# Kernel tuning notes

Hardware: AMD Instinct MI355X
Metric: run time of the kernel (lower is better)

Reference implementation:

```python
import jax, jax.numpy as jnp
import numpy as np

NUM_ITERATIONS = 3
EPS = 1e-8


def squash(s):
    # Hinton squash over the pose dims (last two axes). s: [b, C, os0, os1]
    sq_norm = jnp.sum(s * s, axis=(-2, -1), keepdims=True)
    norm = jnp.sqrt(sq_norm + EPS)
    return (sq_norm / (1.0 + sq_norm)) * (s / norm)


def setup_inputs() -> dict:
    key = jax.random.key(0)
    k1, k2, k3 = jax.random.split(key, 3)
    b, B, H, W = 256, 32, 6, 6
    C, os0, is0 = 10, 16, 16
    input_caps_poses = jax.random.normal(k1, (b, B, H, W, is0, 1), dtype=jnp.float32)
    input_caps_activations = jax.random.uniform(k2, (b, B, H, W), dtype=jnp.float32)
    # weight: [input_caps_types, kh, kw, output_caps_types, os0, is0], std=0.1
    weight = 0.1 * jax.random.normal(k3, (B, H, W, C, os0, is0), dtype=jnp.float32)
    # routing_bias: [C, oh=1, ow=1, os0, os1] initialized to 0.1
    routing_bias = jnp.full((C, 1, 1, os0, 1), 0.1, dtype=jnp.float32)
    return {
        "input_caps_poses": input_caps_poses,
        "input_caps_activations": input_caps_activations,
        "weight": weight,
        "routing_bias": routing_bias,
    }


def reference(input_caps_poses, input_caps_activations, weight, routing_bias):
    # Votes: per input capsule (type B, spatial h,w), transform pose [is0,1]
    # by W[B,h,w,C,os0,is0] -> vote [os0,1] for each output type C.
    # votes: [b, C, B, H, W, os0, os1]
    votes = jnp.einsum('Bhwcoi,bBhwij->bcBhwoj', weight, input_caps_poses)
    b, C, B, H, W, os0, os1 = votes.shape
    bias = routing_bias.reshape(C, os0, os1)  # oh=ow=1

    # Dynamic routing-by-agreement. logits: [b, C, B, H, W]
    logits = jnp.zeros((b, C, B, H, W), dtype=votes.dtype)
    v = None
    c = None
    for it in range(NUM_ITERATIONS):
        c = jax.nn.softmax(logits, axis=1)  # coupling over output types C
        s = jnp.einsum('bcBhw,bcBhwoj->bcoj', c, votes) + bias  # [b,C,os0,os1]
        v = squash(s)
        if it < NUM_ITERATIONS - 1:
            # agreement between output pose and each vote
            logits = logits + jnp.einsum('bcoj,bcBhwoj->bcBhw', v, votes)

    output_caps_poses = v[:, :, None, None]  # [b, C, 1, 1, os0, os1]
    output_caps_activations = jnp.sqrt(
        jnp.sum(v * v, axis=(-2, -1)) + EPS
    )[:, :, None, None]  # [b, C, 1, 1]
    coupling_coefficients = c[:, :, None, None]  # [b, C, 1, 1, B, H, W]
    return (output_caps_poses, output_caps_activations, coupling_coefficients)
```

## Files before the change

### kernel.cpp

```cpp
#include <hip/hip_runtime.h>


#define NPOS 1152
#define NC 10
#define OS 16
#define IS 16
#define NB 256
#define CO (NC * OS)
#define CAPS_EPS 1e-8f
#define PW 9
#define PBLK (NPOS / (4 * PW))
#define NA_SLOTS (NPOS * NC * 32)
#define NB_SLOTS (NPOS * 16 * 32)

typedef __attribute__((ext_vector_type(8))) short bf16x8;
typedef __attribute__((ext_vector_type(4))) float floatx4;

__device__ __forceinline__ unsigned f2bf_rne(float x) {
    union { float f; unsigned u; } v; v.f = x;
    return (v.u + 0x7FFFu + ((v.u >> 16) & 1u)) >> 16;
}

__device__ __forceinline__ bf16x8 pack8(float4 a, float4 b) {
    union { unsigned u[4]; bf16x8 v; } r;
    r.u[0] = f2bf_rne(a.x) | (f2bf_rne(a.y) << 16);
    r.u[1] = f2bf_rne(a.z) | (f2bf_rne(a.w) << 16);
    r.u[2] = f2bf_rne(b.x) | (f2bf_rne(b.y) << 16);
    r.u[3] = f2bf_rne(b.z) | (f2bf_rne(b.w) << 16);
    return r.v;
}

__device__ __forceinline__ bf16x8 zero8() {
    union { unsigned u[4]; bf16x8 v; } r;
    r.u[0] = r.u[1] = r.u[2] = r.u[3] = 0u;
    return r.v;
}

__device__ __forceinline__ bf16x8 load8(const uint4* p) {
    union { uint4 u; bf16x8 v; } r; r.u = *p; return r.v;
}

__global__ __launch_bounds__(256) void preconv_kernel(
    const float* __restrict__ poses, const float* __restrict__ weight,
    uint4* __restrict__ wsA, uint4* __restrict__ wsB)
{
    const int gid = blockIdx.x * 256 + threadIdx.x;
    if (gid < NA_SLOTS) {
        const int L = gid & 31, pc = gid >> 5;
        const int o = L & 15, q = L >> 4;
        const float4* src = (const float4*)(weight + (size_t)pc * 256 + o * 16 + q * 8);
        uint4 d; union { uint4 u; bf16x8 v; } cv;
        cv.v = pack8(src[0], src[1]); d = cv.u;
        wsA[gid] = d;
    } else {
        const int s = gid - NA_SLOTS;
        if (s < NB_SLOTS) {
            const int L = s & 31, pb = s >> 5;
            const int bt = pb & 15, p = pb >> 4;
            const int bl = L & 15, q = L >> 4;
            const float4* src = (const float4*)(poses +
                ((size_t)(bt * 16 + bl) * NPOS + p) * IS + q * 8);
            union { uint4 u; bf16x8 v; } cv;
            cv.v = pack8(src[0], src[1]);
            wsB[s] = cv.u;
        }
    }
}

template <bool PC>
__global__ __launch_bounds__(256, 3) void caps_votes_mfma(
    const float* __restrict__ poses, const float* __restrict__ weight,
    const uint4* __restrict__ wsA, const uint4* __restrict__ wsB,
    const float* __restrict__ vsum, float* __restrict__ sbuf,
    float* __restrict__ out_coup, int it)
{
    const int t    = threadIdx.x;
    const int wave = t >> 6, lane = t & 63;
    const int bcol = lane & 15, quad = lane >> 4;
    const int bt   = blockIdx.y;
    const int b0   = bt * 16;
    const int pbase = blockIdx.x * (4 * PW) + wave * PW;

    __shared__ float s_lds[16 * 161];
    for (int k = t; k < 16 * 161; k += 256) s_lds[k] = 0.f;

    float vs[NC][4];
    if (it > 0) {
        const float* vp = vsum + (size_t)(b0 + bcol) * CO + quad * 4;
#pragma unroll
        for (int c = 0; c < NC; ++c)
#pragma unroll
            for (int r = 0; r < 4; ++r) vs[c][r] = vp[c * 16 + r];
    }
    __syncthreads();

    floatx4 sacc[NC];
#pragma unroll
    for (int c = 0; c < NC; ++c) sacc[c] = (floatx4)(0.f);

    for (int pi = 0; pi < PW; ++pi) {
        const int p = pbase + pi;

        bf16x8 bfrag;
        if (lane < 32) {
            if (PC) {
                bfrag = load8(wsB + ((size_t)p * 16 + bt) * 32 + lane);
            } else {
                const float4* src = (const float4*)(poses +
                    ((size_t)(b0 + bcol) * NPOS + p) * IS + quad * 8);
                bfrag = pack8(src[0], src[1]);
            }
        } else bfrag = zero8();

        if (it == 0) {
#pragma unroll
            for (int c = 0; c < NC; ++c) {
                bf16x8 afrag;
                if (lane < 32) {
                    if (PC) afrag = load8(wsA + ((size_t)p * NC + c) * 32 + lane);
                    else {
                        const float4* src = (const float4*)(weight +
                            (size_t)(p * NC + c) * 256 + bcol * 16 + quad * 8);
                        afrag = pack8(src[0], src[1]);
                    }
                } else afrag = zero8();
                sacc[c] = __builtin_amdgcn_mfma_f32_16x16x32_bf16(afrag, bfrag, sacc[c], 0, 0, 0);
            }
        } else {
            floatx4 acc[NC];
#pragma unroll
            for (int c = 0; c < NC; ++c) {
                bf16x8 afrag;
                if (lane < 32) {
                    if (PC) afrag = load8(wsA + ((size_t)p * NC + c) * 32 + lane);
                    else {
                        const float4* src = (const float4*)(weight +
                            (size_t)(p * NC + c) * 256 + bcol * 16 + quad * 8);
                        afrag = pack8(src[0], src[1]);
                    }
                } else afrag = zero8();
                acc[c] = __builtin_amdgcn_mfma_f32_16x16x32_bf16(afrag, bfrag, (floatx4)(0.f), 0, 0, 0);
            }

            float lg[NC];
            float mx = -1e30f;
#pragma unroll
            for (int c = 0; c < NC; ++c) {
                float pt = vs[c][0] * acc[c][0] + vs[c][1] * acc[c][1]
                         + vs[c][2] * acc[c][2] + vs[c][3] * acc[c][3];
                pt += __shfl_xor(pt, 16);
                pt += __shfl_xor(pt, 32);
                lg[c] = pt;
                mx = fmaxf(mx, pt);
            }
            float coup[NC];
            float sum = 0.f;
#pragma unroll
            for (int c = 0; c < NC; ++c) { coup[c] = __expf(lg[c] - mx); sum += coup[c]; }
            const float inv = 1.f / sum;
#pragma unroll
            for (int c = 0; c < NC; ++c) coup[c] *= inv;

            if (it == 2 && quad == 0) {
                float* cp = out_coup + (size_t)(b0 + bcol) * (NC * NPOS) + p;
#pragma unroll
                for (int c = 0; c < NC; ++c) cp[c * NPOS] = coup[c];
            }

#pragma unroll
            for (int c = 0; c < NC; ++c)
#pragma unroll
                for (int r = 0; r < 4; ++r) sacc[c][r] += coup[c] * acc[c][r];
        }
    }

    const float scale = (it == 0) ? 0.1f : 1.f;
#pragma unroll
    for (int c = 0; c < NC; ++c)
#pragma unroll
        for (int r = 0; r < 4; ++r)
            atomicAdd(&s_lds[bcol * 161 + c * 16 + quad * 4 + r], scale * sacc[c][r]);
    __syncthreads();
    for (int k = t; k < 16 * CO; k += 256) {
        const int b = k / CO, j = k - b * CO;
        unsafeAtomicAdd(&sbuf[(size_t)(b0 + b) * CO + j], s_lds[b * 161 + j]);
    }
}

__global__ __launch_bounds__(256) void caps_squash_kernel(
    const float* __restrict__ rbias,
    float* __restrict__ sbuf,
    float* __restrict__ vsum,
    float* __restrict__ out_poses,
    float* __restrict__ out_act,
    int it)
{
    const int b = blockIdx.x;
    const int t = threadIdx.x;
    if (t >= CO) return;
    const int c = t >> 4;

    const size_t idx = (size_t)b * CO + t;
    const float s = sbuf[idx] + rbias[t];
    float sq = s * s;
    sq += __shfl_xor(sq, 1);
    sq += __shfl_xor(sq, 2);
    sq += __shfl_xor(sq, 4);
    sq += __shfl_xor(sq, 8);
    const float f = (sq / (1.f + sq)) * rsqrtf(sq + CAPS_EPS);
    const float v = f * s;

    if (it < 2) {
        vsum[idx] += v;
        sbuf[idx] = 0.f;
    } else {
        out_poses[idx] = v;
        if ((t & 15) == 0) out_act[(size_t)b * NC + c] = sqrtf(f * f * sq + CAPS_EPS);
    }
}

extern "C" void kernel_launch(void* const* d_in, const int* in_sizes, int n_in,
                              void* d_out, int out_size, void* d_ws, size_t ws_size,
                              hipStream_t stream) {
    const float* poses  = (const float*)d_in[0];
    const float* weight = (const float*)d_in[2];
    const float* rbias  = (const float*)d_in[3];

    float* out       = (float*)d_out;
    float* out_poses = out;
    float* out_act   = out + (size_t)NB * CO;
    float* out_coup  = out_act + (size_t)NB * NC;

    float* sbuf = (float*)d_ws;
    float* vsum = sbuf + (size_t)NB * CO;
    char*  wsfrag = (char*)d_ws + (size_t)2 * NB * CO * sizeof(float);
    uint4* wsA = (uint4*)wsfrag;
    uint4* wsB = wsA + NA_SLOTS;

    const size_t need = (size_t)2 * NB * CO * sizeof(float)
                      + (size_t)(NA_SLOTS + NB_SLOTS) * sizeof(uint4);
    const bool preconv = (ws_size >= need);

    hipMemsetAsync(d_ws, 0, (size_t)2 * NB * CO * sizeof(float), stream);

    if (preconv) {
        hipLaunchKernelGGL(preconv_kernel,
                           dim3((NA_SLOTS + NB_SLOTS) / 256), dim3(256), 0, stream,
                           poses, weight, wsA, wsB);
    }

    for (int it = 0; it < 3; ++it) {
        if (preconv) {
            hipLaunchKernelGGL((caps_votes_mfma<true>), dim3(PBLK, 16), dim3(256), 0, stream,
                               poses, weight, wsA, wsB, vsum, sbuf, out_coup, it);
        } else {
            hipLaunchKernelGGL((caps_votes_mfma<false>), dim3(PBLK, 16), dim3(256), 0, stream,
                               poses, weight, wsA, wsB, vsum, sbuf, out_coup, it);
        }
        hipLaunchKernelGGL(caps_squash_kernel, dim3(NB), dim3(256), 0, stream,
                           rbias, sbuf, vsum, out_poses, out_act, it);
    }
}
```

Baseline: 262.4 us.

## Replace global atomic reduction with per-block partial sums and shrink position tile

```diff
diff --git a/kernel.cpp b/kernel.cpp
--- a/kernel.cpp
+++ b/kernel.cpp
@@ -8,7 +8,7 @@
 #define NB 256
 #define CO (NC * OS)
 #define CAPS_EPS 1e-8f
-#define PW 9
+#define PW 3
 #define PBLK (NPOS / (4 * PW))
 #define NA_SLOTS (NPOS * NC * 32)
 #define NB_SLOTS (NPOS * 16 * 32)
@@ -67,7 +67,7 @@
     }
 }
 
-template <bool PC>
+template <bool PC, bool PART>
 __global__ __launch_bounds__(256, 3) void caps_votes_mfma(
     const float* __restrict__ poses, const float* __restrict__ weight,
     const uint4* __restrict__ wsA, const uint4* __restrict__ wsB,
@@ -181,9 +181,18 @@
         for (int r = 0; r < 4; ++r)
             atomicAdd(&s_lds[bcol * 161 + c * 16 + quad * 4 + r], scale * sacc[c][r]);
     __syncthreads();
-    for (int k = t; k < 16 * CO; k += 256) {
-        const int b = k / CO, j = k - b * CO;
-        unsafeAtomicAdd(&sbuf[(size_t)(b0 + b) * CO + j], s_lds[b * 161 + j]);
+
+    if (PART) {
+        float* pp = sbuf + ((size_t)blockIdx.x * NB + b0) * CO;
+        for (int k = t; k < 16 * CO; k += 256) {
+            const int b = k / CO, j = k - b * CO;
+            pp[(size_t)b * CO + j] = s_lds[b * 161 + j];
+        }
+    } else {
+        for (int k = t; k < 16 * CO; k += 256) {
+            const int b = k / CO, j = k - b * CO;
+            unsafeAtomicAdd(&sbuf[(size_t)(b0 + b) * CO + j], s_lds[b * 161 + j]);
+        }
     }
 }
 
@@ -193,7 +202,7 @@
     float* __restrict__ vsum,
     float* __restrict__ out_poses,
     float* __restrict__ out_act,
-    int it)
+    int it, int npart)
 {
     const int b = blockIdx.x;
     const int t = threadIdx.x;
@@ -201,7 +210,24 @@
     const int c = t >> 4;
 
     const size_t idx = (size_t)b * CO + t;
-    const float s = sbuf[idx] + rbias[t];
+    float s;
+    if (npart > 0) {
+        const float* p = sbuf + idx;
+        const size_t stride = (size_t)NB * CO;
+        float a0 = 0.f, a1 = 0.f, a2 = 0.f, a3 = 0.f;
+        int px = 0;
+        for (; px + 4 <= npart; px += 4) {
+            a0 += p[(size_t)(px + 0) * stride];
+            a1 += p[(size_t)(px + 1) * stride];
+            a2 += p[(size_t)(px + 2) * stride];
+            a3 += p[(size_t)(px + 3) * stride];
+        }
+        for (; px < npart; ++px) a0 += p[(size_t)px * stride];
+        s = ((a0 + a1) + (a2 + a3)) + rbias[t];
+    } else {
+        s = sbuf[idx] + rbias[t];
+    }
+
     float sq = s * s;
     sq += __shfl_xor(sq, 1);
     sq += __shfl_xor(sq, 2);
@@ -212,7 +238,7 @@
 
     if (it < 2) {
         vsum[idx] += v;
-        sbuf[idx] = 0.f;
+        if (npart == 0) sbuf[idx] = 0.f;
     } else {
         out_poses[idx] = v;
         if ((t & 15) == 0) out_act[(size_t)b * NC + c] = sqrtf(f * f * sq + CAPS_EPS);
@@ -231,17 +257,28 @@
     float* out_act   = out + (size_t)NB * CO;
     float* out_coup  = out_act + (size_t)NB * NC;
 
-    float* sbuf = (float*)d_ws;
-    float* vsum = sbuf + (size_t)NB * CO;
-    char*  wsfrag = (char*)d_ws + (size_t)2 * NB * CO * sizeof(float);
-    uint4* wsA = (uint4*)wsfrag;
+    const size_t part_bytes = (size_t)PBLK * NB * CO * sizeof(float);
+    const size_t vsum_bytes = (size_t)NB * CO * sizeof(float);
+    const size_t frag_bytes = (size_t)(NA_SLOTS + NB_SLOTS) * sizeof(uint4);
+
+    const bool part_ok = (ws_size >= part_bytes + vsum_bytes);
+    const bool preconv = (ws_size >= part_bytes + vsum_bytes + frag_bytes);
+
+    float* sbuf;
+    float* vsum;
+    uint4* wsA;
+    if (part_ok) {
+        sbuf = (float*)d_ws;
+        vsum = sbuf + (size_t)PBLK * NB * CO;
+        wsA  = (uint4*)((char*)d_ws + part_bytes + vsum_bytes);
+        hipMemsetAsync(vsum, 0, vsum_bytes, stream);
+    } else {
+        sbuf = (float*)d_ws;
+        vsum = sbuf + (size_t)NB * CO;
+        wsA  = (uint4*)((char*)d_ws + 2 * vsum_bytes);
+        hipMemsetAsync(d_ws, 0, 2 * vsum_bytes, stream);
+    }
     uint4* wsB = wsA + NA_SLOTS;
-
-    const size_t need = (size_t)2 * NB * CO * sizeof(float)
-                      + (size_t)(NA_SLOTS + NB_SLOTS) * sizeof(uint4);
-    const bool preconv = (ws_size >= need);
-
-    hipMemsetAsync(d_ws, 0, (size_t)2 * NB * CO * sizeof(float), stream);
 
     if (preconv) {
         hipLaunchKernelGGL(preconv_kernel,
@@ -251,13 +288,17 @@
 
     for (int it = 0; it < 3; ++it) {
         if (preconv) {
-            hipLaunchKernelGGL((caps_votes_mfma<true>), dim3(PBLK, 16), dim3(256), 0, stream,
+            hipLaunchKernelGGL((caps_votes_mfma<true, true>), dim3(PBLK, 16), dim3(256), 0, stream,
+                               poses, weight, wsA, wsB, vsum, sbuf, out_coup, it);
+        } else if (part_ok) {
+            hipLaunchKernelGGL((caps_votes_mfma<false, true>), dim3(PBLK, 16), dim3(256), 0, stream,
                                poses, weight, wsA, wsB, vsum, sbuf, out_coup, it);
         } else {
-            hipLaunchKernelGGL((caps_votes_mfma<false>), dim3(PBLK, 16), dim3(256), 0, stream,
+            hipLaunchKernelGGL((caps_votes_mfma<false, false>), dim3(PBLK, 16), dim3(256), 0, stream,
                                poses, weight, wsA, wsB, vsum, sbuf, out_coup, it);
         }
         hipLaunchKernelGGL(caps_squash_kernel, dim3(NB), dim3(256), 0, stream,
-                           rbias, sbuf, vsum, out_poses, out_act, it);
-    }
-}
+                           rbias, sbuf, vsum, out_poses, out_act, it,
+                           part_ok ? PBLK : 0);
+    }
+}
```

New measurement: 425.0 us. 1.62x slower.
